# Kernel optimization log

Measured on AMD Instinct MI355X. Metric: run time of the kernel, lower is better.

## Reference

```python
import jax, jax.numpy as jnp
import numpy as np

N = 20000      # nodes
E = 320000     # directed edges (self-loops added inside reference)
DIN = 128      # input_dim
HID = 64       # hidden_dim
H = 4          # num_heads
B = 16         # graphs in batch
OUT = 1        # output_dim
NEG_SLOPE = 0.2


def setup_inputs() -> dict:
    key = jax.random.key(0)
    ks = jax.random.split(key, 20)
    p = lambda k, shape: (jax.random.normal(k, shape, jnp.float32) * 0.05)
    x = jax.random.normal(ks[0], (N, DIN), jnp.float32)
    edge_index = jax.random.randint(ks[1], (2, E), 0, N, dtype=jnp.int64)
    batch = jnp.sort(jax.random.randint(ks[2], (N,), 0, B, dtype=jnp.int64))
    return {
        "x": x, "edge_index": edge_index, "batch": batch,
        # gat1: DIN -> (H, HID), concat
        "W1": p(ks[3], (DIN, H * HID)), "as1": p(ks[4], (H, HID)), "ad1": p(ks[5], (H, HID)), "b1": jnp.zeros((H * HID,), jnp.float32),
        # gat2: H*HID -> (H, HID), concat
        "W2": p(ks[6], (H * HID, H * HID)), "as2": p(ks[7], (H, HID)), "ad2": p(ks[8], (H, HID)), "b2": jnp.zeros((H * HID,), jnp.float32),
        # gat_out: H*HID -> (1, HID), mean (concat=False)
        "W3": p(ks[9], (H * HID, HID)), "as3": p(ks[10], (1, HID)), "ad3": p(ks[11], (1, HID)), "b3": jnp.zeros((HID,), jnp.float32),
        "wp": p(ks[12], (HID, 1)), "bp": jnp.zeros((1,), jnp.float32),
        "wr": p(ks[13], (HID, OUT)), "br": jnp.zeros((OUT,), jnp.float32),
    }


def _gat_layer(x, W, a_src, a_dst, bias, src, dst, heads, concat):
    n = x.shape[0]
    h = (x @ W).reshape(n, heads, -1)                      # [N,H,C]
    e_src = (h * a_src).sum(-1)                            # [N,H]
    e_dst = (h * a_dst).sum(-1)                            # [N,H]
    e = jax.nn.leaky_relu(e_src[src] + e_dst[dst], NEG_SLOPE)  # [Etot,H]
    # segment softmax over destination node (self-loops guarantee non-empty)
    m = jax.ops.segment_max(e, dst, num_segments=n)
    e = jnp.exp(e - m[dst])
    den = jax.ops.segment_sum(e, dst, num_segments=n)
    alpha = e / den[dst]                                   # [Etot,H]
    out = jax.ops.segment_sum(h[src] * alpha[..., None], dst, num_segments=n)  # [N,H,C]
    out = out.reshape(n, -1) if concat else out.mean(axis=1)
    return out + bias


def reference(x, edge_index, batch, W1, as1, ad1, b1, W2, as2, ad2, b2,
              W3, as3, ad3, b3, wp, bp, wr, br):
    n = x.shape[0]
    loops = jnp.arange(n, dtype=edge_index.dtype)
    src = jnp.concatenate([edge_index[0], loops])
    dst = jnp.concatenate([edge_index[1], loops])

    h = jax.nn.elu(_gat_layer(x, W1, as1, ad1, b1, src, dst, H, True))
    h = jax.nn.elu(_gat_layer(h, W2, as2, ad2, b2, src, dst, H, True))
    h = jax.nn.elu(_gat_layer(h, W3, as3, ad3, b3, src, dst, 1, False))  # [N,HID]

    attn = jax.nn.sigmoid(h @ wp + bp)                     # [N,1]
    hw = h * attn                                          # [N,HID]
    sums = jax.ops.segment_sum(hw, batch, num_segments=B)  # [B,HID]
    counts = jax.ops.segment_sum(jnp.ones((n,), hw.dtype), batch, num_segments=B)
    pooled = sums / jnp.maximum(counts, 1.0)[:, None]
    return pooled @ wr + br                                # [B,OUT]
```

## Files before the change

kernel.cpp:

```cpp
#include <hip/hip_runtime.h>


typedef unsigned short u16;
typedef __attribute__((ext_vector_type(8))) short bf16x8;
typedef __attribute__((ext_vector_type(4))) float f32x4;

__device__ __forceinline__ u16 bf16rn(float x) {
    unsigned u = __float_as_uint(x);
    u += 0x7FFFu + ((u >> 16) & 1u);
    return (u16)(u >> 16);
}
__device__ __forceinline__ float bf16f(u16 h) {
    return __uint_as_float(((unsigned)h) << 16);
}

__device__ __forceinline__ void gload16(const u16* g, u16* l) {
    __builtin_amdgcn_global_load_lds(
        (const __attribute__((address_space(1))) unsigned int*)g,
        (__attribute__((address_space(3))) unsigned int*)l, 16, 0, 0);
}

__global__ void edge_hist_k(const int* __restrict__ ei, int E, int n, int* __restrict__ deg) {
    int i = blockIdx.x * blockDim.x + threadIdx.x;
    if (i >= E + n) return;
    int dst = (i < E) ? ei[E + i] : (i - E);
    atomicAdd(&deg[dst], 1);
}

__global__ __launch_bounds__(1024) void scan_excl_k(const int* __restrict__ deg, int* __restrict__ rowptr,
                                                    int* __restrict__ cursor, int n) {
    __shared__ int part[1024];
    int tid = threadIdx.x;
    int chunk = (n + 1023) / 1024;
    int lo = tid * chunk;
    int hi = lo + chunk;
    if (lo > n) lo = n;
    if (hi > n) hi = n;
    int s = 0;
    for (int i = lo; i < hi; ++i) s += deg[i];
    part[tid] = s;
    __syncthreads();
    for (int off = 1; off < 1024; off <<= 1) {
        int v = (tid >= off) ? part[tid - off] : 0;
        __syncthreads();
        part[tid] += v;
        __syncthreads();
    }
    int run = (tid == 0) ? 0 : part[tid - 1];
    for (int i = lo; i < hi; ++i) {
        rowptr[i] = run;
        cursor[i] = run;
        run += deg[i];
    }
    if (tid == 1023) rowptr[n] = run;
}

__global__ void edge_scatter_k(const int* __restrict__ ei, int E, int n,
                               int* __restrict__ cursor, int* __restrict__ srcs) {
    int i = blockIdx.x * blockDim.x + threadIdx.x;
    if (i >= E + n) return;
    int src, dst;
    if (i < E) { src = ei[i]; dst = ei[E + i]; }
    else       { src = i - E; dst = src; }
    int pos = atomicAdd(&cursor[dst], 1);
    srcs[pos] = src;
}

__global__ void split_bf16_k(const float* __restrict__ in, u16* __restrict__ hi,
                             u16* __restrict__ lo, int n4) {
    int i = blockIdx.x * 256 + threadIdx.x;
    if (i >= n4) return;
    float4 v = reinterpret_cast<const float4*>(in)[i];
    u16 hx = bf16rn(v.x), hy = bf16rn(v.y), hz = bf16rn(v.z), hw = bf16rn(v.w);
    ushort4 H = make_ushort4(hx, hy, hz, hw);
    ushort4 L = make_ushort4(bf16rn(v.x - bf16f(hx)), bf16rn(v.y - bf16f(hy)),
                             bf16rn(v.z - bf16f(hz)), bf16rn(v.w - bf16f(hw)));
    reinterpret_cast<ushort4*>(hi)[i] = H;
    reinterpret_cast<ushort4*>(lo)[i] = L;
}

__global__ void splitT_bf16_k(const float* __restrict__ W, u16* __restrict__ thi,
                              u16* __restrict__ tlo, int K, int Nn) {
    int idx = blockIdx.x * 256 + threadIdx.x;
    if (idx >= K * Nn) return;
    int k = idx / Nn, nn = idx - k * Nn;
    float v = W[idx];
    u16 h = bf16rn(v);
    u16 l = bf16rn(v - bf16f(h));
    thi[(size_t)nn * K + k] = h;
    tlo[(size_t)nn * K + k] = l;
}

template <int NF>
__global__ __launch_bounds__(256) void gemm_lds_k(
        const u16* __restrict__ Ahi, const u16* __restrict__ Alo,
        const u16* __restrict__ Bthi, const u16* __restrict__ Btlo,
        float* __restrict__ C,
        const float* __restrict__ a_src, const float* __restrict__ a_dst,
        float* __restrict__ esrc, float* __restrict__ edst,
        int M, int Nn, int K) {
    __shared__ u16 Ah[2][4][64 * 8];
    __shared__ u16 Al[2][4][64 * 8];
    const int mb = (M + 63) >> 6;
    const int mi = blockIdx.x % mb;
    const int ni = blockIdx.x / mb;
    const int m0 = mi * 64;
    const int n0 = ni * (NF * 64);
    const int tid = threadIdx.x;
    const int wv = tid >> 6;
    const int lane = tid & 63;
    const int rr = lane & 15;
    const int kg = lane >> 4;

    int srow = m0 + lane; if (srow > M - 1) srow = M - 1;
    const u16* sh = Ahi + (size_t)srow * K + wv * 8;
    const u16* sl = Alo + (size_t)srow * K + wv * 8;

    const u16* pbh[NF];
    const u16* pbl[NF];
#pragma unroll
    for (int nf = 0; nf < NF; ++nf) {
        int col = n0 + (wv * NF + nf) * 16 + rr;
        pbh[nf] = Bthi + (size_t)col * K + kg * 8;
        pbl[nf] = Btlo + (size_t)col * K + kg * 8;
    }

    f32x4 acc[4][NF];
#pragma unroll
    for (int mf = 0; mf < 4; ++mf)
#pragma unroll
        for (int nf = 0; nf < NF; ++nf) acc[mf][nf] = (f32x4){0.f, 0.f, 0.f, 0.f};

    bf16x8 bhc[NF], blc[NF], bhn[NF], bln[NF];
#pragma unroll
    for (int nf = 0; nf < NF; ++nf) {
        bhc[nf] = *reinterpret_cast<const bf16x8*>(pbh[nf]);
        blc[nf] = *reinterpret_cast<const bf16x8*>(pbl[nf]);
    }
    gload16(sh, &Ah[0][wv][0]);
    gload16(sl, &Al[0][wv][0]);
    __syncthreads();

    const int NT = K >> 5;
    for (int t = 0; t < NT; ++t) {
        const int cur = t & 1;
        if (t + 1 < NT) {
            const int kc = (t + 1) << 5;
#pragma unroll
            for (int nf = 0; nf < NF; ++nf) {
                bhn[nf] = *reinterpret_cast<const bf16x8*>(pbh[nf] + kc);
                bln[nf] = *reinterpret_cast<const bf16x8*>(pbl[nf] + kc);
            }
            gload16(sh + kc, &Ah[cur ^ 1][wv][0]);
            gload16(sl + kc, &Al[cur ^ 1][wv][0]);
        }
        bf16x8 ah[4], al[4];
#pragma unroll
        for (int mf = 0; mf < 4; ++mf) {
            ah[mf] = *reinterpret_cast<const bf16x8*>(&Ah[cur][kg][(mf * 16 + rr) * 8]);
            al[mf] = *reinterpret_cast<const bf16x8*>(&Al[cur][kg][(mf * 16 + rr) * 8]);
        }
#pragma unroll
        for (int mf = 0; mf < 4; ++mf)
#pragma unroll
            for (int nf = 0; nf < NF; ++nf) {
                acc[mf][nf] = __builtin_amdgcn_mfma_f32_16x16x32_bf16(ah[mf], bhc[nf], acc[mf][nf], 0, 0, 0);
                acc[mf][nf] = __builtin_amdgcn_mfma_f32_16x16x32_bf16(ah[mf], blc[nf], acc[mf][nf], 0, 0, 0);
                acc[mf][nf] = __builtin_amdgcn_mfma_f32_16x16x32_bf16(al[mf], bhc[nf], acc[mf][nf], 0, 0, 0);
            }
#pragma unroll
        for (int nf = 0; nf < NF; ++nf) { bhc[nf] = bhn[nf]; blc[nf] = bln[nf]; }
        __syncthreads();
    }

#pragma unroll
    for (int mf = 0; mf < 4; ++mf)
#pragma unroll
        for (int nf = 0; nf < NF; ++nf)
#pragma unroll
            for (int rg = 0; rg < 4; ++rg) {
                int row = m0 + mf * 16 + kg * 4 + rg;
                if (row < M)
                    C[(size_t)row * Nn + n0 + (wv * NF + nf) * 16 + rr] = acc[mf][nf][rg];
            }

    float asv[NF], adv[NF];
#pragma unroll
    for (int nf = 0; nf < NF; ++nf) {
        int col = n0 + (wv * NF + nf) * 16 + rr;
        asv[nf] = a_src[col];
        adv[nf] = a_dst[col];
    }
    float ps[4][4], pd[4][4];
#pragma unroll
    for (int mf = 0; mf < 4; ++mf)
#pragma unroll
        for (int rg = 0; rg < 4; ++rg) {
            float s = 0.f, dvv = 0.f;
#pragma unroll
            for (int nf = 0; nf < NF; ++nf) {
                s = fmaf(acc[mf][nf][rg], asv[nf], s);
                dvv = fmaf(acc[mf][nf][rg], adv[nf], dvv);
            }
#pragma unroll
            for (int off = 1; off < 16; off <<= 1) {
                s += __shfl_xor(s, off);
                dvv += __shfl_xor(dvv, off);
            }
            ps[mf][rg] = s;
            pd[mf][rg] = dvv;
        }
    float* sm_src = (float*)&Ah[0][0][0];
    float* sm_dst = sm_src + 256;
    if (rr == 0) {
#pragma unroll
        for (int mf = 0; mf < 4; ++mf)
#pragma unroll
            for (int rg = 0; rg < 4; ++rg) {
                int rl = mf * 16 + kg * 4 + rg;
                sm_src[wv * 64 + rl] = ps[mf][rg];
                sm_dst[wv * 64 + rl] = pd[mf][rg];
            }
    }
    __syncthreads();
    if (tid < 64) {
        int row = m0 + tid;
        if (row < M) {
            const int HTOT = Nn >> 6;
            constexpr int WPH = 4 / NF;
#pragma unroll
            for (int hl = 0; hl < NF; ++hl) {
                float es = 0.f, edv = 0.f;
#pragma unroll
                for (int w = 0; w < WPH; ++w) {
                    es += sm_src[(hl * WPH + w) * 64 + tid];
                    edv += sm_dst[(hl * WPH + w) * 64 + tid];
                }
                int hg = ni * NF + hl;
                esrc[(size_t)row * HTOT + hg] = es;
                edst[(size_t)row * HTOT + hg] = edv;
            }
        }
    }
}

__global__ __launch_bounds__(256) void gat_aggregate4_k(
        const float* __restrict__ hin, const float* __restrict__ esrc,
        const float* __restrict__ edst, const int* __restrict__ rowptr,
        const int* __restrict__ srcs, const float* __restrict__ bias,
        u16* __restrict__ ghi, u16* __restrict__ glo, int n) {
    int d = blockIdx.x * 4 + (threadIdx.x >> 6);
    int lane = threadIdx.x & 63;
    if (d >= n) return;
    const int hh = lane >> 4;
    const int jj = lane & 15;
    float ed = edst[d * 4 + hh];
    int lo = rowptr[d], hi = rowptr[d + 1];
    float4 acc = make_float4(0.f, 0.f, 0.f, 0.f);
    float den = 0.f;
    for (int base = lo; base < hi; base += 32) {
        int cnt = min(32, hi - base);
        int i0 = base + jj, i1 = base + 16 + jj;
        int s0 = srcs[(i0 < hi) ? i0 : lo];
        int s1 = srcs[(i1 < hi) ? i1 : lo];
        float e0 = esrc[s0 * 4 + hh] + ed;
        e0 = (e0 >= 0.f) ? e0 : 0.2f * e0;
        float w0 = (jj < cnt) ? __expf(e0) : 0.f;
        float e1 = esrc[s1 * 4 + hh] + ed;
        e1 = (e1 >= 0.f) ? e1 : 0.2f * e1;
        float w1 = (jj + 16 < cnt) ? __expf(e1) : 0.f;
        float ws = w0 + w1;
#pragma unroll
        for (int off = 1; off < 16; off <<= 1) ws += __shfl_xor(ws, off);
        den += ws;
        auto loadrow = [&](int j) -> float4 {
            j = (j < cnt) ? j : (cnt - 1);
            int sp = __shfl((j < 16) ? s0 : s1, j & 15);
            return *reinterpret_cast<const float4*>(&hin[(size_t)sp * 256 + lane * 4]);
        };
        auto wsel = [&](int j) -> float {
            return __shfl((j < 16) ? w0 : w1, (lane & 48) | (j & 15));
        };
        float4 p0 = loadrow(0), p1 = loadrow(1), p2 = loadrow(2), p3 = loadrow(3);
        float4 p4 = loadrow(4), p5 = loadrow(5), p6 = loadrow(6), p7 = loadrow(7);
        for (int j = 0; j < cnt; j += 8) {
            float4 q0 = p0, q1 = p1, q2 = p2, q3 = p3;
            float4 q4 = p4, q5 = p5, q6 = p6, q7 = p7;
            p0 = loadrow(j + 8);  p1 = loadrow(j + 9);
            p2 = loadrow(j + 10); p3 = loadrow(j + 11);
            p4 = loadrow(j + 12); p5 = loadrow(j + 13);
            p6 = loadrow(j + 14); p7 = loadrow(j + 15);
            float wA = wsel(j),     wB = wsel(j + 1), wC = wsel(j + 2), wD = wsel(j + 3);
            float wE = wsel(j + 4), wF = wsel(j + 5), wG = wsel(j + 6), wH = wsel(j + 7);
            acc.x = fmaf(wA, q0.x, acc.x); acc.y = fmaf(wA, q0.y, acc.y);
            acc.z = fmaf(wA, q0.z, acc.z); acc.w = fmaf(wA, q0.w, acc.w);
            acc.x = fmaf(wB, q1.x, acc.x); acc.y = fmaf(wB, q1.y, acc.y);
            acc.z = fmaf(wB, q1.z, acc.z); acc.w = fmaf(wB, q1.w, acc.w);
            acc.x = fmaf(wC, q2.x, acc.x); acc.y = fmaf(wC, q2.y, acc.y);
            acc.z = fmaf(wC, q2.z, acc.z); acc.w = fmaf(wC, q2.w, acc.w);
            acc.x = fmaf(wD, q3.x, acc.x); acc.y = fmaf(wD, q3.y, acc.y);
            acc.z = fmaf(wD, q3.z, acc.z); acc.w = fmaf(wD, q3.w, acc.w);
            acc.x = fmaf(wE, q4.x, acc.x); acc.y = fmaf(wE, q4.y, acc.y);
            acc.z = fmaf(wE, q4.z, acc.z); acc.w = fmaf(wE, q4.w, acc.w);
            acc.x = fmaf(wF, q5.x, acc.x); acc.y = fmaf(wF, q5.y, acc.y);
            acc.z = fmaf(wF, q5.z, acc.z); acc.w = fmaf(wF, q5.w, acc.w);
            acc.x = fmaf(wG, q6.x, acc.x); acc.y = fmaf(wG, q6.y, acc.y);
            acc.z = fmaf(wG, q6.z, acc.z); acc.w = fmaf(wG, q6.w, acc.w);
            acc.x = fmaf(wH, q7.x, acc.x); acc.y = fmaf(wH, q7.y, acc.y);
            acc.z = fmaf(wH, q7.z, acc.z); acc.w = fmaf(wH, q7.w, acc.w);
        }
    }
    float inv = 1.f / den;
    float4 bv = *reinterpret_cast<const float4*>(&bias[lane * 4]);
    float4 o;
    o.x = acc.x * inv + bv.x;
    o.y = acc.y * inv + bv.y;
    o.z = acc.z * inv + bv.z;
    o.w = acc.w * inv + bv.w;
    o.x = (o.x > 0.f) ? o.x : expm1f(o.x);
    o.y = (o.y > 0.f) ? o.y : expm1f(o.y);
    o.z = (o.z > 0.f) ? o.z : expm1f(o.z);
    o.w = (o.w > 0.f) ? o.w : expm1f(o.w);
    u16 hx = bf16rn(o.x), hy = bf16rn(o.y), hz = bf16rn(o.z), hw = bf16rn(o.w);
    ushort4 H = make_ushort4(hx, hy, hz, hw);
    ushort4 L = make_ushort4(bf16rn(o.x - bf16f(hx)), bf16rn(o.y - bf16f(hy)),
                             bf16rn(o.z - bf16f(hz)), bf16rn(o.w - bf16f(hw)));
    *reinterpret_cast<ushort4*>(&ghi[(size_t)d * 256 + lane * 4]) = H;
    *reinterpret_cast<ushort4*>(&glo[(size_t)d * 256 + lane * 4]) = L;
}

__global__ __launch_bounds__(256) void gat_aggregate1_attn_k(
        const float* __restrict__ hin, const float* __restrict__ esrc,
        const float* __restrict__ edst, const int* __restrict__ rowptr,
        const int* __restrict__ srcs, const float* __restrict__ bias,
        const float* __restrict__ wp, const float* __restrict__ bp,
        float* __restrict__ gout, float* __restrict__ attn, int n) {
    int d = blockIdx.x * 4 + (threadIdx.x >> 6);
    int lane = threadIdx.x & 63;
    if (d >= n) return;
    float ed = edst[d];
    int lo = rowptr[d], hi = rowptr[d + 1];
    float den = 0.f, acc = 0.f;
    for (int base = lo; base < hi; base += 64) {
        int cnt = min(64, hi - base);
        int idx = base + lane;
        int s = srcs[(idx < hi) ? idx : lo];
        float e = esrc[s] + ed;
        e = (e >= 0.f) ? e : 0.2f * e;
        float w = (lane < cnt) ? __expf(e) : 0.f;
        float ws = w;
#pragma unroll
        for (int off = 1; off < 64; off <<= 1) ws += __shfl_xor(ws, off);
        den += ws;
        auto loadrow = [&](int j) -> float {
            j = (j < cnt) ? j : (cnt - 1);
            int sp = __shfl(s, j);
            return hin[(size_t)sp * 64 + lane];
        };
        float p0 = loadrow(0), p1 = loadrow(1), p2 = loadrow(2), p3 = loadrow(3);
        float p4 = loadrow(4), p5 = loadrow(5), p6 = loadrow(6), p7 = loadrow(7);
        for (int j = 0; j < cnt; j += 8) {
            float q0 = p0, q1 = p1, q2 = p2, q3 = p3;
            float q4 = p4, q5 = p5, q6 = p6, q7 = p7;
            p0 = loadrow(j + 8);  p1 = loadrow(j + 9);
            p2 = loadrow(j + 10); p3 = loadrow(j + 11);
            p4 = loadrow(j + 12); p5 = loadrow(j + 13);
            p6 = loadrow(j + 14); p7 = loadrow(j + 15);
            acc = fmaf(__shfl(w, j), q0, acc);
            acc = fmaf(__shfl(w, j + 1), q1, acc);
            acc = fmaf(__shfl(w, j + 2), q2, acc);
            acc = fmaf(__shfl(w, j + 3), q3, acc);
            acc = fmaf(__shfl(w, j + 4), q4, acc);
            acc = fmaf(__shfl(w, j + 5), q5, acc);
            acc = fmaf(__shfl(w, j + 6), q6, acc);
            acc = fmaf(__shfl(w, j + 7), q7, acc);
        }
    }
    float o = acc / den + bias[lane];
    o = (o > 0.f) ? o : expm1f(o);
    gout[(size_t)d * 64 + lane] = o;
    float v = o * wp[lane];
#pragma unroll
    for (int off = 32; off; off >>= 1) v += __shfl_xor(v, off);
    if (lane == 0) attn[d] = 1.f / (1.f + __expf(-(v + bp[0])));
}

__global__ void pool_partial_k(const float* __restrict__ g3, const float* __restrict__ attn,
                               const int* __restrict__ batch, int n, float* __restrict__ sums) {
    int wid = blockIdx.x * (blockDim.x >> 6) + (threadIdx.x >> 6);
    int lane = threadIdx.x & 63;
    int nwaves = gridDim.x * (blockDim.x >> 6);
    int per = (n + nwaves - 1) / nwaves;
    int i0 = wid * per;
    int i1 = i0 + per;
    if (i1 > n) i1 = n;
    if (i0 >= i1) return;
    int cur = batch[i0];
    float acc = 0.f;
    for (int i = i0; i < i1; ++i) {
        int b = batch[i];
        if (b != cur) {
            atomicAdd(&sums[cur * 64 + lane], acc);
            acc = 0.f;
            cur = b;
        }
        acc += g3[(size_t)i * 64 + lane] * attn[i];
    }
    atomicAdd(&sums[cur * 64 + lane], acc);
}

__global__ void regress_k(const float* __restrict__ sums, const int* __restrict__ batch, int n,
                          const float* __restrict__ wr, const float* __restrict__ br,
                          float* __restrict__ out, int B) {
    int b = threadIdx.x >> 6;
    int lane = threadIdx.x & 63;
    if (b >= B) return;
    int lo = 0, hi = n;
    while (lo < hi) { int mid = (lo + hi) >> 1; if (batch[mid] < b) lo = mid + 1; else hi = mid; }
    int seg_lo = lo;
    lo = 0; hi = n;
    while (lo < hi) { int mid = (lo + hi) >> 1; if (batch[mid] < b + 1) lo = mid + 1; else hi = mid; }
    float cnt = (float)(lo - seg_lo);
    if (cnt < 1.f) cnt = 1.f;
    float v = (sums[b * 64 + lane] / cnt) * wr[lane];
#pragma unroll
    for (int off = 32; off; off >>= 1) v += __shfl_xor(v, off);
    if (lane == 0) out[b] = v + br[0];
}

extern "C" void kernel_launch(void* const* d_in, const int* in_sizes, int n_in,
                              void* d_out, int out_size, void* d_ws, size_t ws_size,
                              hipStream_t stream) {
    const float* x   = (const float*)d_in[0];
    const int*   ei  = (const int*)d_in[1];
    const int*   bat = (const int*)d_in[2];
    const float* W1  = (const float*)d_in[3];
    const float* as1 = (const float*)d_in[4];
    const float* ad1 = (const float*)d_in[5];
    const float* b1  = (const float*)d_in[6];
    const float* W2  = (const float*)d_in[7];
    const float* as2 = (const float*)d_in[8];
    const float* ad2 = (const float*)d_in[9];
    const float* b2  = (const float*)d_in[10];
    const float* W3  = (const float*)d_in[11];
    const float* as3 = (const float*)d_in[12];
    const float* ad3 = (const float*)d_in[13];
    const float* b3  = (const float*)d_in[14];
    const float* wp  = (const float*)d_in[15];
    const float* bp  = (const float*)d_in[16];
    const float* wr  = (const float*)d_in[17];
    const float* br  = (const float*)d_in[18];
    float* out = (float*)d_out;

    const int N    = in_sizes[2];
    const int E    = in_sizes[1] / 2;
    const int DIN  = in_sizes[0] / N;
    const int Etot = E + N;
    const int Bc   = out_size;

    char* ws = (char*)d_ws;
    size_t off = 0;
    auto alloc = [&](size_t bytes) {
        void* p = ws + off;
        off = (off + bytes + 255) & ~(size_t)255;
        return p;
    };
    int*   deg    = (int*)alloc((size_t)N * 4);
    int*   rowptr = (int*)alloc((size_t)(N + 1) * 4);
    int*   cursor = (int*)alloc((size_t)N * 4);
    int*   srcs   = (int*)alloc((size_t)Etot * 4);
    float* bufA   = (float*)alloc((size_t)N * 256 * 4);
    u16*   Ahi    = (u16*)alloc((size_t)N * 256 * 2);
    u16*   Alo    = (u16*)alloc((size_t)N * 256 * 2);
    float* h3     = (float*)alloc((size_t)N * 64 * 4);
    float* g3     = (float*)alloc((size_t)N * 64 * 4);
    float* esrc   = (float*)alloc((size_t)N * 4 * 4);
    float* edst   = (float*)alloc((size_t)N * 4 * 4);
    float* attn   = (float*)alloc((size_t)N * 4);
    float* sums   = (float*)alloc((size_t)Bc * 64 * 4);
    u16*   w1hi   = (u16*)alloc((size_t)256 * DIN * 2);
    u16*   w1lo   = (u16*)alloc((size_t)256 * DIN * 2);
    u16*   w2hi   = (u16*)alloc((size_t)256 * 256 * 2);
    u16*   w2lo   = (u16*)alloc((size_t)256 * 256 * 2);
    u16*   w3hi   = (u16*)alloc((size_t)64 * 256 * 2);
    u16*   w3lo   = (u16*)alloc((size_t)64 * 256 * 2);
    (void)ws_size;

    hipMemsetAsync(deg, 0, (size_t)N * 4, stream);
    int eb = (Etot + 255) / 256;
    edge_hist_k<<<eb, 256, 0, stream>>>(ei, E, N, deg);
    scan_excl_k<<<1, 1024, 0, stream>>>(deg, rowptr, cursor, N);
    edge_scatter_k<<<eb, 256, 0, stream>>>(ei, E, N, cursor, srcs);

    splitT_bf16_k<<<(DIN * 256 + 255) / 256, 256, 0, stream>>>(W1, w1hi, w1lo, DIN, 256);
    splitT_bf16_k<<<(256 * 256 + 255) / 256, 256, 0, stream>>>(W2, w2hi, w2lo, 256, 256);
    splitT_bf16_k<<<(256 * 64 + 255) / 256, 256, 0, stream>>>(W3, w3hi, w3lo, 256, 64);
    split_bf16_k<<<(N * DIN / 4 + 255) / 256, 256, 0, stream>>>(x, Ahi, Alo, N * DIN / 4);

    const int mb = (N + 63) / 64;
    int nb4 = (N + 3) / 4;

    gemm_lds_k<2><<<mb * 2, 256, 0, stream>>>(Ahi, Alo, w1hi, w1lo, bufA, as1, ad1, esrc, edst, N, 256, DIN);
    gat_aggregate4_k<<<nb4, 256, 0, stream>>>(bufA, esrc, edst, rowptr, srcs, b1, Ahi, Alo, N);

    gemm_lds_k<2><<<mb * 2, 256, 0, stream>>>(Ahi, Alo, w2hi, w2lo, bufA, as2, ad2, esrc, edst, N, 256, 256);
    gat_aggregate4_k<<<nb4, 256, 0, stream>>>(bufA, esrc, edst, rowptr, srcs, b2, Ahi, Alo, N);

    gemm_lds_k<1><<<mb, 256, 0, stream>>>(Ahi, Alo, w3hi, w3lo, h3, as3, ad3, esrc, edst, N, 64, 256);
    gat_aggregate1_attn_k<<<nb4, 256, 0, stream>>>(h3, esrc, edst, rowptr, srcs, b3, wp, bp, g3, attn, N);

    hipMemsetAsync(sums, 0, (size_t)Bc * 64 * 4, stream);
    pool_partial_k<<<256, 256, 0, stream>>>(g3, attn, bat, N, sums);
    regress_k<<<1, 1024, 0, stream>>>(sums, bat, N, wr, br, out, Bc);
}
```

Baseline: 277.3 us.

## Store GEMM output head-major and aggregate each head in its own grid slice

The GEMM epilogue now writes features head-major, as [head][node][64], instead of row-major [node][256]. The aggregation kernel becomes one wave per (node, head), with the head taken from blockIdx.y. Each lane handles one feature of that head with scalar loads, and a 64-lane shuffle reduction replaces the 16-lane groups. The aim is a more compact per-head gather footprint, better cache locality per head slice, and more waves in flight. In exchange, the edge list, scores and softmax weights are recomputed once per head, and each gathered row is a 256-byte scalar load instead of a 1 KB float4 load.

```diff
diff --git a/kernel.cpp b/kernel.cpp
--- a/kernel.cpp
+++ b/kernel.cpp
@@ -176,13 +176,15 @@
 #pragma unroll
     for (int mf = 0; mf < 4; ++mf)
 #pragma unroll
-        for (int nf = 0; nf < NF; ++nf)
+        for (int nf = 0; nf < NF; ++nf) {
+            int col = n0 + (wv * NF + nf) * 16 + rr;
+            float* cb = C + ((size_t)(col >> 6) * M) * 64 + (col & 63);
 #pragma unroll
             for (int rg = 0; rg < 4; ++rg) {
                 int row = m0 + mf * 16 + kg * 4 + rg;
-                if (row < M)
-                    C[(size_t)row * Nn + n0 + (wv * NF + nf) * 16 + rr] = acc[mf][nf][rg];
-            }
+                if (row < M) cb[(size_t)row * 64] = acc[mf][nf][rg];
+            }
+        }
 
     float asv[NF], adv[NF];
 #pragma unroll
@@ -244,89 +246,60 @@
     }
 }
 
-__global__ __launch_bounds__(256) void gat_aggregate4_k(
-        const float* __restrict__ hin, const float* __restrict__ esrc,
+__global__ __launch_bounds__(256) void gat_aggregate_hm_k(
+        const float* __restrict__ hm, const float* __restrict__ esrc,
         const float* __restrict__ edst, const int* __restrict__ rowptr,
         const int* __restrict__ srcs, const float* __restrict__ bias,
         u16* __restrict__ ghi, u16* __restrict__ glo, int n) {
     int d = blockIdx.x * 4 + (threadIdx.x >> 6);
     int lane = threadIdx.x & 63;
+    int hh = blockIdx.y;
     if (d >= n) return;
-    const int hh = lane >> 4;
-    const int jj = lane & 15;
+    const float* hbase = hm + (size_t)hh * n * 64;
     float ed = edst[d * 4 + hh];
     int lo = rowptr[d], hi = rowptr[d + 1];
-    float4 acc = make_float4(0.f, 0.f, 0.f, 0.f);
-    float den = 0.f;
-    for (int base = lo; base < hi; base += 32) {
-        int cnt = min(32, hi - base);
-        int i0 = base + jj, i1 = base + 16 + jj;
-        int s0 = srcs[(i0 < hi) ? i0 : lo];
-        int s1 = srcs[(i1 < hi) ? i1 : lo];
-        float e0 = esrc[s0 * 4 + hh] + ed;
-        e0 = (e0 >= 0.f) ? e0 : 0.2f * e0;
-        float w0 = (jj < cnt) ? __expf(e0) : 0.f;
-        float e1 = esrc[s1 * 4 + hh] + ed;
-        e1 = (e1 >= 0.f) ? e1 : 0.2f * e1;
-        float w1 = (jj + 16 < cnt) ? __expf(e1) : 0.f;
-        float ws = w0 + w1;
-#pragma unroll
-        for (int off = 1; off < 16; off <<= 1) ws += __shfl_xor(ws, off);
+    float den = 0.f, acc = 0.f;
+    for (int base = lo; base < hi; base += 64) {
+        int cnt = min(64, hi - base);
+        int idx = base + lane;
+        int s = srcs[(idx < hi) ? idx : lo];
+        float e = esrc[s * 4 + hh] + ed;
+        e = (e >= 0.f) ? e : 0.2f * e;
+        float w = (lane < cnt) ? __expf(e) : 0.f;
+        float ws = w;
+#pragma unroll
+        for (int off = 1; off < 64; off <<= 1) ws += __shfl_xor(ws, off);
         den += ws;
-        auto loadrow = [&](int j) -> float4 {
+        auto loadrow = [&](int j) -> float {
             j = (j < cnt) ? j : (cnt - 1);
-            int sp = __shfl((j < 16) ? s0 : s1, j & 15);
-            return *reinterpret_cast<const float4*>(&hin[(size_t)sp * 256 + lane * 4]);
+            int sp = __shfl(s, j);
+            return hbase[(size_t)sp * 64 + lane];
         };
-        auto wsel = [&](int j) -> float {
-            return __shfl((j < 16) ? w0 : w1, (lane & 48) | (j & 15));
-        };
-        float4 p0 = loadrow(0), p1 = loadrow(1), p2 = loadrow(2), p3 = loadrow(3);
-        float4 p4 = loadrow(4), p5 = loadrow(5), p6 = loadrow(6), p7 = loadrow(7);
+        float p0 = loadrow(0), p1 = loadrow(1), p2 = loadrow(2), p3 = loadrow(3);
+        float p4 = loadrow(4), p5 = loadrow(5), p6 = loadrow(6), p7 = loadrow(7);
         for (int j = 0; j < cnt; j += 8) {
-            float4 q0 = p0, q1 = p1, q2 = p2, q3 = p3;
-            float4 q4 = p4, q5 = p5, q6 = p6, q7 = p7;
+            float q0 = p0, q1 = p1, q2 = p2, q3 = p3;
+            float q4 = p4, q5 = p5, q6 = p6, q7 = p7;
             p0 = loadrow(j + 8);  p1 = loadrow(j + 9);
             p2 = loadrow(j + 10); p3 = loadrow(j + 11);
             p4 = loadrow(j + 12); p5 = loadrow(j + 13);
             p6 = loadrow(j + 14); p7 = loadrow(j + 15);
-            float wA = wsel(j),     wB = wsel(j + 1), wC = wsel(j + 2), wD = wsel(j + 3);
-            float wE = wsel(j + 4), wF = wsel(j + 5), wG = wsel(j + 6), wH = wsel(j + 7);
-            acc.x = fmaf(wA, q0.x, acc.x); acc.y = fmaf(wA, q0.y, acc.y);
-            acc.z = fmaf(wA, q0.z, acc.z); acc.w = fmaf(wA, q0.w, acc.w);
-            acc.x = fmaf(wB, q1.x, acc.x); acc.y = fmaf(wB, q1.y, acc.y);
-            acc.z = fmaf(wB, q1.z, acc.z); acc.w = fmaf(wB, q1.w, acc.w);
-            acc.x = fmaf(wC, q2.x, acc.x); acc.y = fmaf(wC, q2.y, acc.y);
-            acc.z = fmaf(wC, q2.z, acc.z); acc.w = fmaf(wC, q2.w, acc.w);
-            acc.x = fmaf(wD, q3.x, acc.x); acc.y = fmaf(wD, q3.y, acc.y);
-            acc.z = fmaf(wD, q3.z, acc.z); acc.w = fmaf(wD, q3.w, acc.w);
-            acc.x = fmaf(wE, q4.x, acc.x); acc.y = fmaf(wE, q4.y, acc.y);
-            acc.z = fmaf(wE, q4.z, acc.z); acc.w = fmaf(wE, q4.w, acc.w);
-            acc.x = fmaf(wF, q5.x, acc.x); acc.y = fmaf(wF, q5.y, acc.y);
-            acc.z = fmaf(wF, q5.z, acc.z); acc.w = fmaf(wF, q5.w, acc.w);
-            acc.x = fmaf(wG, q6.x, acc.x); acc.y = fmaf(wG, q6.y, acc.y);
-            acc.z = fmaf(wG, q6.z, acc.z); acc.w = fmaf(wG, q6.w, acc.w);
-            acc.x = fmaf(wH, q7.x, acc.x); acc.y = fmaf(wH, q7.y, acc.y);
-            acc.z = fmaf(wH, q7.z, acc.z); acc.w = fmaf(wH, q7.w, acc.w);
-        }
-    }
-    float inv = 1.f / den;
-    float4 bv = *reinterpret_cast<const float4*>(&bias[lane * 4]);
-    float4 o;
-    o.x = acc.x * inv + bv.x;
-    o.y = acc.y * inv + bv.y;
-    o.z = acc.z * inv + bv.z;
-    o.w = acc.w * inv + bv.w;
-    o.x = (o.x > 0.f) ? o.x : expm1f(o.x);
-    o.y = (o.y > 0.f) ? o.y : expm1f(o.y);
-    o.z = (o.z > 0.f) ? o.z : expm1f(o.z);
-    o.w = (o.w > 0.f) ? o.w : expm1f(o.w);
-    u16 hx = bf16rn(o.x), hy = bf16rn(o.y), hz = bf16rn(o.z), hw = bf16rn(o.w);
-    ushort4 H = make_ushort4(hx, hy, hz, hw);
-    ushort4 L = make_ushort4(bf16rn(o.x - bf16f(hx)), bf16rn(o.y - bf16f(hy)),
-                             bf16rn(o.z - bf16f(hz)), bf16rn(o.w - bf16f(hw)));
-    *reinterpret_cast<ushort4*>(&ghi[(size_t)d * 256 + lane * 4]) = H;
-    *reinterpret_cast<ushort4*>(&glo[(size_t)d * 256 + lane * 4]) = L;
+            acc = fmaf(__shfl(w, j), q0, acc);
+            acc = fmaf(__shfl(w, j + 1), q1, acc);
+            acc = fmaf(__shfl(w, j + 2), q2, acc);
+            acc = fmaf(__shfl(w, j + 3), q3, acc);
+            acc = fmaf(__shfl(w, j + 4), q4, acc);
+            acc = fmaf(__shfl(w, j + 5), q5, acc);
+            acc = fmaf(__shfl(w, j + 6), q6, acc);
+            acc = fmaf(__shfl(w, j + 7), q7, acc);
+        }
+    }
+    int c = hh * 64 + lane;
+    float o = acc / den + bias[c];
+    o = (o > 0.f) ? o : expm1f(o);
+    u16 oh = bf16rn(o);
+    ghi[(size_t)d * 256 + c] = oh;
+    glo[(size_t)d * 256 + c] = bf16rn(o - bf16f(oh));
 }
 
 __global__ __launch_bounds__(256) void gat_aggregate1_attn_k(
@@ -499,12 +472,13 @@
 
     const int mb = (N + 63) / 64;
     int nb4 = (N + 3) / 4;
+    dim3 agg_grid(nb4, 4);
 
     gemm_lds_k<2><<<mb * 2, 256, 0, stream>>>(Ahi, Alo, w1hi, w1lo, bufA, as1, ad1, esrc, edst, N, 256, DIN);
-    gat_aggregate4_k<<<nb4, 256, 0, stream>>>(bufA, esrc, edst, rowptr, srcs, b1, Ahi, Alo, N);
+    gat_aggregate_hm_k<<<agg_grid, 256, 0, stream>>>(bufA, esrc, edst, rowptr, srcs, b1, Ahi, Alo, N);
 
     gemm_lds_k<2><<<mb * 2, 256, 0, stream>>>(Ahi, Alo, w2hi, w2lo, bufA, as2, ad2, esrc, edst, N, 256, 256);
-    gat_aggregate4_k<<<nb4, 256, 0, stream>>>(bufA, esrc, edst, rowptr, srcs, b2, Ahi, Alo, N);
+    gat_aggregate_hm_k<<<agg_grid, 256, 0, stream>>>(bufA, esrc, edst, rowptr, srcs, b2, Ahi, Alo, N);
 
     gemm_lds_k<1><<<mb, 256, 0, stream>>>(Ahi, Alo, w3hi, w3lo, h3, as3, ad3, esrc, edst, N, 64, 256);
     gat_aggregate1_attn_k<<<nb4, 256, 0, stream>>>(h3, esrc, edst, rowptr, srcs, b3, wp, bp, g3, attn, N);
```

New measurement: 284.6 us. 2.6% more time.
